# Kernel optimization log

Hardware: AMD Instinct MI355X
Metric: run time of the kernel (lower is better)

Reference implementation:

```python
import jax, jax.numpy as jnp
import numpy as np

N_NODES = 349525  # complete 4-ary tree, depth 10: (4**10 - 1) / 3
X_SIZE = 128
H_SIZE = 128


def setup_inputs() -> dict:
    key = jax.random.key(0)
    ks = jax.random.split(key, 6)
    s = 0.05  # keep gates out of saturation
    return {
        "x": jax.random.normal(ks[0], (N_NODES, X_SIZE), jnp.float32),
        "W_iou": jax.random.normal(ks[1], (X_SIZE, 3 * H_SIZE), jnp.float32) * s,
        "U_iou": jax.random.normal(ks[2], (H_SIZE, 3 * H_SIZE), jnp.float32) * s,
        "b_iou": jnp.zeros((3 * H_SIZE,), jnp.float32),
        "W_f": jax.random.normal(ks[3], (X_SIZE, H_SIZE), jnp.float32) * s,
        "U_f": jax.random.normal(ks[4], (H_SIZE, H_SIZE), jnp.float32) * s,
        "b_f": jnp.zeros((H_SIZE,), jnp.float32),
        "depth": 10,
        "branching": 4,
    }


def _apply_node(iou, c_sum):
    # apply_node_func: i,o,u gates then cell/hidden update
    i, o, u = jnp.split(iou, 3, axis=-1)
    c = jax.nn.sigmoid(i) * jnp.tanh(u) + c_sum
    h = jax.nn.sigmoid(o) * jnp.tanh(c)
    return h, c


def reference(x, W_iou, U_iou, b_iou, W_f, U_f, b_f, depth, branching):
    # Nodes are in BFS order of a complete `branching`-ary forest-tree;
    # level l occupies [off[l], off[l+1]) and the children of level l are
    # exactly level l+1 (contiguous, `branching` per parent).
    H = b_f.shape[-1]
    off = [(branching ** l - 1) // (branching - 1) for l in range(depth + 1)]

    node_iou = x @ W_iou + b_iou  # [N, 3H]  (W_iou(x) + b_iou)
    node_f = x @ W_f + b_f        # [N, H]   (W_f(x) + b_f)

    h_levels = [None] * depth
    c_levels = [None] * depth

    # Leaves: mailbox empty -> h_tilda = 0, c = 0
    s, e = off[depth - 1], off[depth]
    h, c = _apply_node(node_iou[s:e], jnp.zeros((e - s, H), x.dtype))
    h_levels[depth - 1], c_levels[depth - 1] = h, c

    # Bottom-up topological propagation
    for l in range(depth - 2, -1, -1):
        s, e = off[l], off[l + 1]
        nl = e - s
        ch_h = h_levels[l + 1].reshape(nl, branching, H)  # mailbox['h']
        ch_c = c_levels[l + 1].reshape(nl, branching, H)  # mailbox['c']
        h_tilda = ch_h.sum(axis=1)
        # f = sigmoid(U_f(mailbox.h) + node_f[:, None])
        f = jax.nn.sigmoid(jnp.einsum("nkh,hg->nkg", ch_h, U_f) + node_f[s:e][:, None, :])
        c_sum = (f * ch_c).sum(axis=1)
        iou = node_iou[s:e] + h_tilda @ U_iou
        h, c = _apply_node(iou, c_sum)
        h_levels[l], c_levels[l] = h, c

    h_all = jnp.concatenate(h_levels, axis=0)
    c_all = jnp.concatenate(c_levels, axis=0)
    return h_all, c_all
```

## Files before the change

### kernel.cpp

```cpp
#include <hip/hip_runtime.h>

#define H 128

typedef __bf16 bf16x8 __attribute__((ext_vector_type(8)));
typedef float f32x4 __attribute__((ext_vector_type(4)));

__device__ __forceinline__ float fsig(float x) { return 1.0f / (1.0f + __expf(-x)); }
__device__ __forceinline__ float ftanh(float x) {
  float ax = fabsf(x), e = __expf(-2.0f * ax);
  float t = (1.0f - e) / (1.0f + e);
  return x < 0.0f ? -t : t;
}
__device__ __forceinline__ uint2 pack4(float a, float b, float c, float d) {
  union { __bf16 h[4]; uint2 u; } r;
  r.h[0] = (__bf16)a; r.h[1] = (__bf16)b; r.h[2] = (__bf16)c; r.h[3] = (__bf16)d;
  return r.u;
}
__device__ __forceinline__ unsigned swz(unsigned row, unsigned colByte, unsigned rowBytes) {
  return (row * rowBytes + colByte) ^ ((row & 7) << 4);
}

__global__ __launch_bounds__(256)
void prep_weights(const float* __restrict__ W_iou, const float* __restrict__ U_iou,
                  const float* __restrict__ W_f, const float* __restrict__ U_f,
                  uint4* __restrict__ ws)
{
  int item = blockIdx.x * 256 + threadIdx.x;
  float v[8];
  if (item < 2048) {
    int fj = item >> 8, rem = item & 255, ks = rem >> 6, lane = rem & 63;
    int n = fj * 16 + (lane & 15), kb = ks * 32 + (lane >> 4) * 8;
    #pragma unroll
    for (int j = 0; j < 8; j++) v[j] = U_f[(kb + j) * H + n];
  } else if (item < 4096) {
    int i2 = item - 2048;
    int fj = i2 >> 8, rem = i2 & 255, ks = rem >> 6, lane = rem & 63;
    int n = fj * 16 + (lane & 15), kb = ks * 32 + (lane >> 4) * 8;
    #pragma unroll
    for (int j = 0; j < 8; j++) v[j] = W_f[(kb + j) * H + n];
  } else {
    int i2 = item - 4096;
    int fj = i2 >> 9, rem = i2 & 511, ks = rem >> 6, lane = rem & 63;
    int col = (fj >> 3) * 128 + (fj & 7) * 16 + (lane & 15);
    int kb = ks * 32 + (lane >> 4) * 8;
    #pragma unroll
    for (int j = 0; j < 8; j++) {
      int k = kb + j;
      v[j] = (k < 128) ? W_iou[k * 384 + col] : U_iou[(k - 128) * 384 + col];
    }
  }
  union { __bf16 h[8]; uint4 u; } r;
  #pragma unroll
  for (int j = 0; j < 8; j++) r.h[j] = (__bf16)v[j];
  ws[item] = r.u;
}

__global__ __launch_bounds__(256)
void leaf3(const float* __restrict__ x, const __bf16* __restrict__ iou_fmt,
           const float* __restrict__ b_iou,
           float* __restrict__ h_glob, float* __restrict__ c_glob, int leaf_start)
{
  __shared__ __align__(16) char As[64 * 256];
  const int t = threadIdx.x;
  const int m0 = leaf_start + blockIdx.x * 64;

  #pragma unroll
  for (int i = 0; i < 8; i++) {
    int idx = t + i * 256;
    int r = idx >> 5, k0 = (idx & 31) << 2;
    f32x4 v = *reinterpret_cast<const f32x4*>(&x[(size_t)(m0 + r) * H + k0]);
    *reinterpret_cast<uint2*>(As + swz(r, k0 * 2, 256)) = pack4(v.x, v.y, v.z, v.w);
  }
  __syncthreads();

  const int lane = t & 63, w = t >> 6;
  const int l15 = lane & 15, l4 = lane >> 4;

  f32x4 acc[4][3][2] = {};
  #pragma unroll
  for (int ks = 0; ks < 4; ks++) {
    bf16x8 a[4], b[3][2];
    #pragma unroll
    for (int m = 0; m < 4; m++)
      a[m] = *reinterpret_cast<const bf16x8*>(As + swz(m * 16 + l15, (ks * 32 + l4 * 8) * 2, 256));
    #pragma unroll
    for (int g = 0; g < 3; g++)
      #pragma unroll
      for (int j = 0; j < 2; j++) {
        int nf = g * 8 + 2 * w + j;
        b[g][j] = *reinterpret_cast<const bf16x8*>(iou_fmt + ((size_t)(nf * 8 + ks) * 64 + lane) * 8);
      }
    #pragma unroll
    for (int m = 0; m < 4; m++)
      #pragma unroll
      for (int g = 0; g < 3; g++)
        #pragma unroll
        for (int j = 0; j < 2; j++)
          acc[m][g][j] = __builtin_amdgcn_mfma_f32_16x16x32_bf16(a[m], b[g][j], acc[m][g][j], 0, 0, 0);
  }

  #pragma unroll
  for (int j = 0; j < 2; j++) {
    int ch = (2 * w + j) * 16 + l15;
    float bi = b_iou[ch], bo = b_iou[H + ch], bu = b_iou[2 * H + ch];
    #pragma unroll
    for (int m = 0; m < 4; m++) {
      int rowb = m * 16 + l4 * 4;
      #pragma unroll
      for (int r = 0; r < 4; r++) {
        size_t o = (size_t)(m0 + rowb + r) * H + ch;
        float c = fsig(acc[m][0][j][r] + bi) * ftanh(acc[m][2][j][r] + bu);
        float h = fsig(acc[m][1][j][r] + bo) * ftanh(c);
        h_glob[o] = h;
        c_glob[o] = c;
      }
    }
  }
}

__global__ __launch_bounds__(256)
void fused_level(const float* __restrict__ x, const __bf16* __restrict__ uf_fmt,
                 const __bf16* __restrict__ wf_fmt, const __bf16* __restrict__ iou_fmt,
                 const float* __restrict__ b_iou, const float* __restrict__ b_f,
                 float* __restrict__ h_glob, float* __restrict__ c_glob,
                 int pstart, int cstart)
{
  __shared__ __align__(16) char CH[128 * 256];
  __shared__ __align__(16) char XH[32 * 512];
  __shared__ float SFX[32][128];
  __shared__ float CSUM[32][128];
  const int t = threadIdx.x;
  const int p0 = blockIdx.x * 32;
  const int c0 = blockIdx.x * 128;

  #pragma unroll
  for (int i = 0; i < 4; i++) {
    int idx = t + i * 256;
    int p = idx >> 5, k0 = (idx & 31) << 2;
    f32x4 s = {};
    #pragma unroll
    for (int j = 0; j < 4; j++) {
      f32x4 v = *reinterpret_cast<const f32x4*>(&h_glob[(size_t)(cstart + c0 + p * 4 + j) * H + k0]);
      *reinterpret_cast<uint2*>(CH + swz(p * 4 + j, k0 * 2, 256)) = pack4(v.x, v.y, v.z, v.w);
      s += v;
    }
    *reinterpret_cast<uint2*>(XH + swz(p, (128 + k0) * 2, 512)) = pack4(s.x, s.y, s.z, s.w);
  }
  #pragma unroll
  for (int i = 0; i < 4; i++) {
    int idx = t + i * 256;
    int p = idx >> 5, k0 = (idx & 31) << 2;
    f32x4 v = *reinterpret_cast<const f32x4*>(&x[(size_t)(pstart + p0 + p) * H + k0]);
    *reinterpret_cast<uint2*>(XH + swz(p, k0 * 2, 512)) = pack4(v.x, v.y, v.z, v.w);
  }
  __syncthreads();

  const int lane = t & 63, w = t >> 6;
  const int l15 = lane & 15, l4 = lane >> 4;

  {
    f32x4 acc[2][2] = {};
    #pragma unroll
    for (int ks = 0; ks < 4; ks++) {
      bf16x8 a[2], b[2];
      #pragma unroll
      for (int m = 0; m < 2; m++)
        a[m] = *reinterpret_cast<const bf16x8*>(XH + swz(m * 16 + l15, (ks * 32 + l4 * 8) * 2, 512));
      #pragma unroll
      for (int n = 0; n < 2; n++) {
        int nf = 2 * w + n;
        b[n] = *reinterpret_cast<const bf16x8*>(wf_fmt + ((size_t)(nf * 4 + ks) * 64 + lane) * 8);
      }
      #pragma unroll
      for (int m = 0; m < 2; m++)
        #pragma unroll
        for (int n = 0; n < 2; n++)
          acc[m][n] = __builtin_amdgcn_mfma_f32_16x16x32_bf16(a[m], b[n], acc[m][n], 0, 0, 0);
    }
    #pragma unroll
    for (int m = 0; m < 2; m++)
      #pragma unroll
      for (int n = 0; n < 2; n++)
        #pragma unroll
        for (int r = 0; r < 4; r++)
          SFX[m * 16 + l4 * 4 + r][(2 * w + n) * 16 + l15] = acc[m][n][r];
  }
  __syncthreads();

  {
    f32x4 acc[2][8] = {};
    #pragma unroll
    for (int ks = 0; ks < 4; ks++) {
      bf16x8 a[2], b[8];
      #pragma unroll
      for (int m = 0; m < 2; m++)
        a[m] = *reinterpret_cast<const bf16x8*>(CH + swz(w * 32 + m * 16 + l15, (ks * 32 + l4 * 8) * 2, 256));
      #pragma unroll
      for (int n = 0; n < 8; n++)
        b[n] = *reinterpret_cast<const bf16x8*>(uf_fmt + ((size_t)(n * 4 + ks) * 64 + lane) * 8);
      #pragma unroll
      for (int m = 0; m < 2; m++)
        #pragma unroll
        for (int n = 0; n < 8; n++)
          acc[m][n] = __builtin_amdgcn_mfma_f32_16x16x32_bf16(a[m], b[n], acc[m][n], 0, 0, 0);
    }
    #pragma unroll
    for (int m = 0; m < 2; m++) {
      int rbase = w * 32 + m * 16 + l4 * 4;
      int ploc = rbase >> 2;
      #pragma unroll
      for (int n = 0; n < 8; n++) {
        int ch = n * 16 + l15;
        float sfx = SFX[ploc][ch] + b_f[ch];
        float cs = 0.0f;
        #pragma unroll
        for (int r = 0; r < 4; r++) {
          float f = fsig(acc[m][n][r] + sfx);
          cs = fmaf(f, c_glob[(size_t)(cstart + c0 + rbase + r) * H + ch], cs);
        }
        CSUM[ploc][ch] = cs;
      }
    }
  }
  __syncthreads();

  {
    f32x4 acc[2][3][2] = {};
    #pragma unroll
    for (int ks = 0; ks < 8; ks++) {
      bf16x8 a[2], b[3][2];
      #pragma unroll
      for (int m = 0; m < 2; m++)
        a[m] = *reinterpret_cast<const bf16x8*>(XH + swz(m * 16 + l15, (ks * 32 + l4 * 8) * 2, 512));
      #pragma unroll
      for (int g = 0; g < 3; g++)
        #pragma unroll
        for (int j = 0; j < 2; j++) {
          int nf = g * 8 + 2 * w + j;
          b[g][j] = *reinterpret_cast<const bf16x8*>(iou_fmt + ((size_t)(nf * 8 + ks) * 64 + lane) * 8);
        }
      #pragma unroll
      for (int m = 0; m < 2; m++)
        #pragma unroll
        for (int g = 0; g < 3; g++)
          #pragma unroll
          for (int j = 0; j < 2; j++)
            acc[m][g][j] = __builtin_amdgcn_mfma_f32_16x16x32_bf16(a[m], b[g][j], acc[m][g][j], 0, 0, 0);
    }
    #pragma unroll
    for (int j = 0; j < 2; j++) {
      int ch = (2 * w + j) * 16 + l15;
      float bi = b_iou[ch], bo = b_iou[H + ch], bu = b_iou[2 * H + ch];
      #pragma unroll
      for (int m = 0; m < 2; m++) {
        #pragma unroll
        for (int r = 0; r < 4; r++) {
          int ploc = m * 16 + l4 * 4 + r;
          float gi = acc[m][0][j][r] + bi;
          float go = acc[m][1][j][r] + bo;
          float gu = acc[m][2][j][r] + bu;
          float cs = CSUM[ploc][ch];
          float c = fsig(gi) * ftanh(gu) + cs;
          float h = fsig(go) * ftanh(c);
          size_t o = (size_t)(pstart + p0 + ploc) * H + ch;
          h_glob[o] = h;
          c_glob[o] = c;
        }
      }
    }
  }
}

#define SNR 4
#define SRP 2
#define BR 4

__global__ __launch_bounds__(256)
void small_kernel(const float* __restrict__ x,
                  const float* __restrict__ W_iou, const float* __restrict__ b_iou,
                  const float* __restrict__ U_iou, const float* __restrict__ W_f,
                  const float* __restrict__ U_f, const float* __restrict__ b_f,
                  float* __restrict__ h_out, float* __restrict__ c_out,
                  int lvl_start, int child_start, int n_lvl)
{
  __shared__ float xs[SNR][H];
  __shared__ float hs[SNR * BR][H];
  __shared__ float ht[SNR][H];
  const int t = threadIdx.x;
  const int node0 = blockIdx.x * SNR;
  const int nrows = min(SNR, n_lvl - node0);

  {
    const f32x4* xgv = reinterpret_cast<const f32x4*>(x + (size_t)(lvl_start + node0) * H);
    f32x4* xsv = reinterpret_cast<f32x4*>(&xs[0][0]);
    int total = nrows * (H / 4);
    for (int i = t; i < total; i += 256) xsv[i] = xgv[i];
  }
  {
    const f32x4* hgv = reinterpret_cast<const f32x4*>(h_out + (size_t)(child_start + node0 * BR) * H);
    f32x4* hsv = reinterpret_cast<f32x4*>(&hs[0][0]);
    int total = nrows * BR * (H / 4);
    for (int i = t; i < total; i += 256) hsv[i] = hgv[i];
  }
  __syncthreads();

  const int ch = t & (H - 1);
  const int g = t >> 7;

  float fx[SRP], ai[SRP], ao[SRP], au[SRP];
  {
    float bi = b_iou[ch], bo = b_iou[ch + H], bu = b_iou[ch + 2 * H], bf = b_f[ch];
    #pragma unroll
    for (int r = 0; r < SRP; r++) { fx[r] = bf; ai[r] = bi; ao[r] = bo; au[r] = bu; }
  }
  {
    const float* wfp = W_f + ch;
    const float* wip = W_iou + ch;
    #pragma unroll 4
    for (int k = 0; k < H; k++) {
      float wf = wfp[k * H];
      float w0 = wip[k * 384], w1 = wip[k * 384 + H], w2 = wip[k * 384 + 2 * H];
      #pragma unroll
      for (int r = 0; r < SRP; r++) {
        float xk = xs[g * SRP + r][k];
        fx[r] = fmaf(xk, wf, fx[r]);
        ai[r] = fmaf(xk, w0, ai[r]);
        ao[r] = fmaf(xk, w1, ao[r]);
        au[r] = fmaf(xk, w2, au[r]);
      }
    }
  }
  #pragma unroll
  for (int r = 0; r < SRP; r++) {
    int row = g * SRP + r;
    float s = hs[row * BR + 0][ch] + hs[row * BR + 1][ch]
            + hs[row * BR + 2][ch] + hs[row * BR + 3][ch];
    ht[row][ch] = s;
  }
  __syncthreads();

  float z[BR][SRP];
  #pragma unroll
  for (int kc = 0; kc < BR; kc++)
    #pragma unroll
    for (int r = 0; r < SRP; r++) z[kc][r] = fx[r];
  {
    const float* ufp = U_f + ch;
    #pragma unroll 4
    for (int m = 0; m < H; m++) {
      float uf = ufp[m * H];
      #pragma unroll
      for (int kc = 0; kc < BR; kc++)
        #pragma unroll
        for (int r = 0; r < SRP; r++)
          z[kc][r] = fmaf(hs[(g * SRP + r) * BR + kc][m], uf, z[kc][r]);
    }
  }
  float csum[SRP];
  #pragma unroll
  for (int r = 0; r < SRP; r++) csum[r] = 0.0f;
  #pragma unroll
  for (int kc = 0; kc < BR; kc++) {
    #pragma unroll
    for (int r = 0; r < SRP; r++) {
      size_t childnode = (size_t)child_start + (size_t)(node0 + g * SRP + r) * BR + kc;
      float f = fsig(z[kc][r]);
      csum[r] = fmaf(f, c_out[childnode * H + ch], csum[r]);
    }
  }
  {
    const float* uip = U_iou + ch;
    #pragma unroll 4
    for (int m = 0; m < H; m++) {
      float w0 = uip[m * 384], w1 = uip[m * 384 + H], w2 = uip[m * 384 + 2 * H];
      #pragma unroll
      for (int r = 0; r < SRP; r++) {
        float hm = ht[g * SRP + r][m];
        ai[r] = fmaf(hm, w0, ai[r]);
        ao[r] = fmaf(hm, w1, ao[r]);
        au[r] = fmaf(hm, w2, au[r]);
      }
    }
  }
  #pragma unroll
  for (int r = 0; r < SRP; r++) {
    int row = g * SRP + r;
    if (row < nrows) {
      float c = fsig(ai[r]) * ftanh(au[r]) + csum[r];
      float h = fsig(ao[r]) * ftanh(c);
      size_t node = (size_t)(lvl_start + node0 + row);
      h_out[node * H + ch] = h;
      c_out[node * H + ch] = c;
    }
  }
}

extern "C" void kernel_launch(void* const* d_in, const int* in_sizes, int n_in,
                              void* d_out, int out_size, void* d_ws, size_t ws_size,
                              hipStream_t stream)
{
  const float* x     = (const float*)d_in[0];
  const float* W_iou = (const float*)d_in[1];
  const float* U_iou = (const float*)d_in[2];
  const float* b_iou = (const float*)d_in[3];
  const float* W_f   = (const float*)d_in[4];
  const float* U_f   = (const float*)d_in[5];
  const float* b_f   = (const float*)d_in[6];
  const int N = 349525;

  float* h_out = (float*)d_out;
  float* c_out = h_out + (size_t)N * H;

  const __bf16* uf_fmt  = (const __bf16*)d_ws;
  const __bf16* wf_fmt  = (const __bf16*)d_ws + 16384;
  const __bf16* iou_fmt = (const __bf16*)d_ws + 32768;

  int off[11];
  off[0] = 0;
  for (int l = 1; l <= 10; l++) off[l] = off[l - 1] * 4 + 1;

  prep_weights<<<64, 256, 0, stream>>>(W_iou, U_iou, W_f, U_f, (uint4*)d_ws);

  leaf3<<<4096, 256, 0, stream>>>(x, iou_fmt, b_iou, h_out, c_out, off[9]);

  for (int l = 8; l >= 5; l--) {
    int n_par = off[l + 1] - off[l];
    fused_level<<<n_par / 32, 256, 0, stream>>>(x, uf_fmt, wf_fmt, iou_fmt, b_iou, b_f,
                                                h_out, c_out, off[l], off[l + 1]);
  }

  for (int l = 4; l >= 0; l--) {
    int s = off[l], e = off[l + 1];
    int n = e - s;
    int grid = (n + SNR - 1) / SNR;
    small_kernel<<<grid, 256, 0, stream>>>(x, W_iou, b_iou, U_iou, W_f, U_f, b_f,
                                           h_out, c_out, s, e, n);
  }
}
```

Baseline: 409.2 us.

## Pipeline leaf tiles with double-buffered LDS, merge shared buffers, fast reciprocals

The leaf kernel now processes four 64-row tiles per block, prefetching the next tile's x into registers while computing the current one and double-buffering LDS. fused_level merges its SFX and CSUM shared arrays into one buffer to cut LDS use and allow more blocks per CU. Sigmoid and tanh use hardware approximate reciprocals instead of divides. Level 4 moves from the small kernel to fused_level. Risks are reduced precision in the gates and fewer blocks for the leaf level.

```diff
diff --git a/kernel.cpp b/kernel.cpp
--- a/kernel.cpp
+++ b/kernel.cpp
@@ -5,10 +5,12 @@
 typedef __bf16 bf16x8 __attribute__((ext_vector_type(8)));
 typedef float f32x4 __attribute__((ext_vector_type(4)));
 
-__device__ __forceinline__ float fsig(float x) { return 1.0f / (1.0f + __expf(-x)); }
+__device__ __forceinline__ float fsig(float x) {
+  return __builtin_amdgcn_rcpf(1.0f + __expf(-x));
+}
 __device__ __forceinline__ float ftanh(float x) {
   float ax = fabsf(x), e = __expf(-2.0f * ax);
-  float t = (1.0f - e) / (1.0f + e);
+  float t = (1.0f - e) * __builtin_amdgcn_rcpf(1.0f + e);
   return x < 0.0f ? -t : t;
 }
 __device__ __forceinline__ uint2 pack4(float a, float b, float c, float d) {
@@ -55,66 +57,88 @@
   ws[item] = r.u;
 }
 
-__global__ __launch_bounds__(256)
-void leaf3(const float* __restrict__ x, const __bf16* __restrict__ iou_fmt,
+#define LTILES 4
+__global__ __launch_bounds__(256, 3)
+void leaf4(const float* __restrict__ x, const __bf16* __restrict__ iou_fmt,
            const float* __restrict__ b_iou,
            float* __restrict__ h_glob, float* __restrict__ c_glob, int leaf_start)
 {
-  __shared__ __align__(16) char As[64 * 256];
+  __shared__ __align__(16) char As[2][64 * 256];
   const int t = threadIdx.x;
-  const int m0 = leaf_start + blockIdx.x * 64;
-
-  #pragma unroll
-  for (int i = 0; i < 8; i++) {
-    int idx = t + i * 256;
-    int r = idx >> 5, k0 = (idx & 31) << 2;
-    f32x4 v = *reinterpret_cast<const f32x4*>(&x[(size_t)(m0 + r) * H + k0]);
-    *reinterpret_cast<uint2*>(As + swz(r, k0 * 2, 256)) = pack4(v.x, v.y, v.z, v.w);
-  }
-  __syncthreads();
-
+  const int m00 = leaf_start + blockIdx.x * (64 * LTILES);
   const int lane = t & 63, w = t >> 6;
   const int l15 = lane & 15, l4 = lane >> 4;
-
-  f32x4 acc[4][3][2] = {};
-  #pragma unroll
-  for (int ks = 0; ks < 4; ks++) {
-    bf16x8 a[4], b[3][2];
-    #pragma unroll
-    for (int m = 0; m < 4; m++)
-      a[m] = *reinterpret_cast<const bf16x8*>(As + swz(m * 16 + l15, (ks * 32 + l4 * 8) * 2, 256));
-    #pragma unroll
-    for (int g = 0; g < 3; g++)
-      #pragma unroll
-      for (int j = 0; j < 2; j++) {
-        int nf = g * 8 + 2 * w + j;
-        b[g][j] = *reinterpret_cast<const bf16x8*>(iou_fmt + ((size_t)(nf * 8 + ks) * 64 + lane) * 8);
-      }
-    #pragma unroll
-    for (int m = 0; m < 4; m++)
+  const int r_st = t >> 5;
+  const int k_st = (t & 31) << 2;
+
+  f32x4 rg[8];
+  #pragma unroll
+  for (int i = 0; i < 8; i++)
+    rg[i] = *reinterpret_cast<const f32x4*>(&x[(size_t)(m00 + r_st + i * 8) * H + k_st]);
+  #pragma unroll
+  for (int i = 0; i < 8; i++)
+    *reinterpret_cast<uint2*>(As[0] + swz(r_st + i * 8, k_st * 2, 256)) =
+        pack4(rg[i].x, rg[i].y, rg[i].z, rg[i].w);
+  __syncthreads();
+
+  for (int tt = 0; tt < LTILES; tt++) {
+    if (tt + 1 < LTILES) {
+      #pragma unroll
+      for (int i = 0; i < 8; i++)
+        rg[i] = *reinterpret_cast<const f32x4*>(
+            &x[(size_t)(m00 + (tt + 1) * 64 + r_st + i * 8) * H + k_st]);
+    }
+    const char* A = As[tt & 1];
+    const int m0 = m00 + tt * 64;
+
+    f32x4 acc[4][3][2] = {};
+    #pragma unroll
+    for (int ks = 0; ks < 4; ks++) {
+      bf16x8 a[4], b[3][2];
+      #pragma unroll
+      for (int m = 0; m < 4; m++)
+        a[m] = *reinterpret_cast<const bf16x8*>(A + swz(m * 16 + l15, (ks * 32 + l4 * 8) * 2, 256));
       #pragma unroll
       for (int g = 0; g < 3; g++)
         #pragma unroll
-        for (int j = 0; j < 2; j++)
-          acc[m][g][j] = __builtin_amdgcn_mfma_f32_16x16x32_bf16(a[m], b[g][j], acc[m][g][j], 0, 0, 0);
-  }
-
-  #pragma unroll
-  for (int j = 0; j < 2; j++) {
-    int ch = (2 * w + j) * 16 + l15;
-    float bi = b_iou[ch], bo = b_iou[H + ch], bu = b_iou[2 * H + ch];
-    #pragma unroll
-    for (int m = 0; m < 4; m++) {
-      int rowb = m * 16 + l4 * 4;
-      #pragma unroll
-      for (int r = 0; r < 4; r++) {
-        size_t o = (size_t)(m0 + rowb + r) * H + ch;
-        float c = fsig(acc[m][0][j][r] + bi) * ftanh(acc[m][2][j][r] + bu);
-        float h = fsig(acc[m][1][j][r] + bo) * ftanh(c);
-        h_glob[o] = h;
-        c_glob[o] = c;
-      }
-    }
+        for (int j = 0; j < 2; j++) {
+          int nf = g * 8 + 2 * w + j;
+          b[g][j] = *reinterpret_cast<const bf16x8*>(iou_fmt + ((size_t)(nf * 8 + ks) * 64 + lane) * 8);
+        }
+      #pragma unroll
+      for (int m = 0; m < 4; m++)
+        #pragma unroll
+        for (int g = 0; g < 3; g++)
+          #pragma unroll
+          for (int j = 0; j < 2; j++)
+            acc[m][g][j] = __builtin_amdgcn_mfma_f32_16x16x32_bf16(a[m], b[g][j], acc[m][g][j], 0, 0, 0);
+    }
+
+    #pragma unroll
+    for (int j = 0; j < 2; j++) {
+      int ch = (2 * w + j) * 16 + l15;
+      float bi = b_iou[ch], bo = b_iou[H + ch], bu = b_iou[2 * H + ch];
+      #pragma unroll
+      for (int m = 0; m < 4; m++) {
+        int rowb = m * 16 + l4 * 4;
+        #pragma unroll
+        for (int r = 0; r < 4; r++) {
+          size_t o = (size_t)(m0 + rowb + r) * H + ch;
+          float c = fsig(acc[m][0][j][r] + bi) * ftanh(acc[m][2][j][r] + bu);
+          float h = fsig(acc[m][1][j][r] + bo) * ftanh(c);
+          h_glob[o] = h;
+          c_glob[o] = c;
+        }
+      }
+    }
+
+    if (tt + 1 < LTILES) {
+      #pragma unroll
+      for (int i = 0; i < 8; i++)
+        *reinterpret_cast<uint2*>(As[(tt + 1) & 1] + swz(r_st + i * 8, k_st * 2, 256)) =
+            pack4(rg[i].x, rg[i].y, rg[i].z, rg[i].w);
+    }
+    __syncthreads();
   }
 }
 
@@ -127,8 +151,7 @@
 {
   __shared__ __align__(16) char CH[128 * 256];
   __shared__ __align__(16) char XH[32 * 512];
-  __shared__ float SFX[32][128];
-  __shared__ float CSUM[32][128];
+  __shared__ float SC[32][128];
   const int t = threadIdx.x;
   const int p0 = blockIdx.x * 32;
   const int c0 = blockIdx.x * 128;
@@ -183,7 +206,7 @@
       for (int n = 0; n < 2; n++)
         #pragma unroll
         for (int r = 0; r < 4; r++)
-          SFX[m * 16 + l4 * 4 + r][(2 * w + n) * 16 + l15] = acc[m][n][r];
+          SC[m * 16 + l4 * 4 + r][(2 * w + n) * 16 + l15] = acc[m][n][r];
   }
   __syncthreads();
 
@@ -211,14 +234,14 @@
       #pragma unroll
       for (int n = 0; n < 8; n++) {
         int ch = n * 16 + l15;
-        float sfx = SFX[ploc][ch] + b_f[ch];
+        float sfx = SC[ploc][ch] + b_f[ch];
         float cs = 0.0f;
         #pragma unroll
         for (int r = 0; r < 4; r++) {
           float f = fsig(acc[m][n][r] + sfx);
           cs = fmaf(f, c_glob[(size_t)(cstart + c0 + rbase + r) * H + ch], cs);
         }
-        CSUM[ploc][ch] = cs;
+        SC[ploc][ch] = cs;
       }
     }
   }
@@ -259,7 +282,7 @@
           float gi = acc[m][0][j][r] + bi;
           float go = acc[m][1][j][r] + bo;
           float gu = acc[m][2][j][r] + bu;
-          float cs = CSUM[ploc][ch];
+          float cs = SC[ploc][ch];
           float c = fsig(gi) * ftanh(gu) + cs;
           float h = fsig(go) * ftanh(c);
           size_t o = (size_t)(pstart + p0 + ploc) * H + ch;
@@ -421,15 +444,15 @@
 
   prep_weights<<<64, 256, 0, stream>>>(W_iou, U_iou, W_f, U_f, (uint4*)d_ws);
 
-  leaf3<<<4096, 256, 0, stream>>>(x, iou_fmt, b_iou, h_out, c_out, off[9]);
-
-  for (int l = 8; l >= 5; l--) {
+  leaf4<<<1024, 256, 0, stream>>>(x, iou_fmt, b_iou, h_out, c_out, off[9]);
+
+  for (int l = 8; l >= 4; l--) {
     int n_par = off[l + 1] - off[l];
     fused_level<<<n_par / 32, 256, 0, stream>>>(x, uf_fmt, wf_fmt, iou_fmt, b_iou, b_f,
                                                 h_out, c_out, off[l], off[l + 1]);
   }
 
-  for (int l = 4; l >= 0; l--) {
+  for (int l = 3; l >= 0; l--) {
     int s = off[l], e = off[l + 1];
     int n = e - s;
     int grid = (n + SNR - 1) / SNR;
```

Result: slower. 558.1 us (+36.4%).

## Trim leaf registers, merge LDS buffers, use rcp intrinsics, fuse level four

Applied to the files above, without the earlier changes.

The leaf kernel now loops over the two column halves without unrolling, which cuts the live MFMA accumulators by half and should lower register pressure and raise occupancy. In fused_level, the SFX and CSUM shared buffers are merged into one array, freeing 16 KB of LDS per block. The divisions in sigmoid and tanh are replaced by the hardware reciprocal intrinsic, which is slightly less accurate. Level 4 now runs through the MFMA fused_level kernel instead of the scalar small kernel, though that level launches only 8 blocks.

```diff
diff --git a/kernel.cpp b/kernel.cpp
--- a/kernel.cpp
+++ b/kernel.cpp
@@ -5,10 +5,12 @@
 typedef __bf16 bf16x8 __attribute__((ext_vector_type(8)));
 typedef float f32x4 __attribute__((ext_vector_type(4)));
 
-__device__ __forceinline__ float fsig(float x) { return 1.0f / (1.0f + __expf(-x)); }
+__device__ __forceinline__ float fsig(float x) {
+  return __builtin_amdgcn_rcpf(1.0f + __expf(-x));
+}
 __device__ __forceinline__ float ftanh(float x) {
   float ax = fabsf(x), e = __expf(-2.0f * ax);
-  float t = (1.0f - e) / (1.0f + e);
+  float t = (1.0f - e) * __builtin_amdgcn_rcpf(1.0f + e);
   return x < 0.0f ? -t : t;
 }
 __device__ __forceinline__ uint2 pack4(float a, float b, float c, float d) {
@@ -56,7 +58,7 @@
 }
 
 __global__ __launch_bounds__(256)
-void leaf3(const float* __restrict__ x, const __bf16* __restrict__ iou_fmt,
+void leaf5(const float* __restrict__ x, const __bf16* __restrict__ iou_fmt,
            const float* __restrict__ b_iou,
            float* __restrict__ h_glob, float* __restrict__ c_glob, int leaf_start)
 {
@@ -76,31 +78,27 @@
   const int lane = t & 63, w = t >> 6;
   const int l15 = lane & 15, l4 = lane >> 4;
 
-  f32x4 acc[4][3][2] = {};
-  #pragma unroll
-  for (int ks = 0; ks < 4; ks++) {
-    bf16x8 a[4], b[3][2];
-    #pragma unroll
-    for (int m = 0; m < 4; m++)
-      a[m] = *reinterpret_cast<const bf16x8*>(As + swz(m * 16 + l15, (ks * 32 + l4 * 8) * 2, 256));
-    #pragma unroll
-    for (int g = 0; g < 3; g++)
-      #pragma unroll
-      for (int j = 0; j < 2; j++) {
+  #pragma unroll 1
+  for (int j = 0; j < 2; j++) {
+    f32x4 acc[4][3] = {};
+    #pragma unroll
+    for (int ks = 0; ks < 4; ks++) {
+      bf16x8 a[4], b[3];
+      #pragma unroll
+      for (int m = 0; m < 4; m++)
+        a[m] = *reinterpret_cast<const bf16x8*>(As + swz(m * 16 + l15, (ks * 32 + l4 * 8) * 2, 256));
+      #pragma unroll
+      for (int g = 0; g < 3; g++) {
         int nf = g * 8 + 2 * w + j;
-        b[g][j] = *reinterpret_cast<const bf16x8*>(iou_fmt + ((size_t)(nf * 8 + ks) * 64 + lane) * 8);
-      }
-    #pragma unroll
-    for (int m = 0; m < 4; m++)
-      #pragma unroll
-      for (int g = 0; g < 3; g++)
-        #pragma unroll
-        for (int j = 0; j < 2; j++)
-          acc[m][g][j] = __builtin_amdgcn_mfma_f32_16x16x32_bf16(a[m], b[g][j], acc[m][g][j], 0, 0, 0);
-  }
-
-  #pragma unroll
-  for (int j = 0; j < 2; j++) {
+        b[g] = *reinterpret_cast<const bf16x8*>(iou_fmt + ((size_t)(nf * 8 + ks) * 64 + lane) * 8);
+      }
+      #pragma unroll
+      for (int m = 0; m < 4; m++)
+        #pragma unroll
+        for (int g = 0; g < 3; g++)
+          acc[m][g] = __builtin_amdgcn_mfma_f32_16x16x32_bf16(a[m], b[g], acc[m][g], 0, 0, 0);
+    }
+
     int ch = (2 * w + j) * 16 + l15;
     float bi = b_iou[ch], bo = b_iou[H + ch], bu = b_iou[2 * H + ch];
     #pragma unroll
@@ -109,8 +107,8 @@
       #pragma unroll
       for (int r = 0; r < 4; r++) {
         size_t o = (size_t)(m0 + rowb + r) * H + ch;
-        float c = fsig(acc[m][0][j][r] + bi) * ftanh(acc[m][2][j][r] + bu);
-        float h = fsig(acc[m][1][j][r] + bo) * ftanh(c);
+        float c = fsig(acc[m][0][r] + bi) * ftanh(acc[m][2][r] + bu);
+        float h = fsig(acc[m][1][r] + bo) * ftanh(c);
         h_glob[o] = h;
         c_glob[o] = c;
       }
@@ -127,8 +125,7 @@
 {
   __shared__ __align__(16) char CH[128 * 256];
   __shared__ __align__(16) char XH[32 * 512];
-  __shared__ float SFX[32][128];
-  __shared__ float CSUM[32][128];
+  __shared__ float SC[32][128];
   const int t = threadIdx.x;
   const int p0 = blockIdx.x * 32;
   const int c0 = blockIdx.x * 128;
@@ -183,7 +180,7 @@
       for (int n = 0; n < 2; n++)
         #pragma unroll
         for (int r = 0; r < 4; r++)
-          SFX[m * 16 + l4 * 4 + r][(2 * w + n) * 16 + l15] = acc[m][n][r];
+          SC[m * 16 + l4 * 4 + r][(2 * w + n) * 16 + l15] = acc[m][n][r];
   }
   __syncthreads();
 
@@ -211,14 +208,14 @@
       #pragma unroll
       for (int n = 0; n < 8; n++) {
         int ch = n * 16 + l15;
-        float sfx = SFX[ploc][ch] + b_f[ch];
+        float sfx = SC[ploc][ch] + b_f[ch];
         float cs = 0.0f;
         #pragma unroll
         for (int r = 0; r < 4; r++) {
           float f = fsig(acc[m][n][r] + sfx);
           cs = fmaf(f, c_glob[(size_t)(cstart + c0 + rbase + r) * H + ch], cs);
         }
-        CSUM[ploc][ch] = cs;
+        SC[ploc][ch] = cs;
       }
     }
   }
@@ -259,7 +256,7 @@
           float gi = acc[m][0][j][r] + bi;
           float go = acc[m][1][j][r] + bo;
           float gu = acc[m][2][j][r] + bu;
-          float cs = CSUM[ploc][ch];
+          float cs = SC[ploc][ch];
           float c = fsig(gi) * ftanh(gu) + cs;
           float h = fsig(go) * ftanh(c);
           size_t o = (size_t)(pstart + p0 + ploc) * H + ch;
@@ -421,15 +418,15 @@
 
   prep_weights<<<64, 256, 0, stream>>>(W_iou, U_iou, W_f, U_f, (uint4*)d_ws);
 
-  leaf3<<<4096, 256, 0, stream>>>(x, iou_fmt, b_iou, h_out, c_out, off[9]);
-
-  for (int l = 8; l >= 5; l--) {
+  leaf5<<<4096, 256, 0, stream>>>(x, iou_fmt, b_iou, h_out, c_out, off[9]);
+
+  for (int l = 8; l >= 4; l--) {
     int n_par = off[l + 1] - off[l];
     fused_level<<<n_par / 32, 256, 0, stream>>>(x, uf_fmt, wf_fmt, iou_fmt, b_iou, b_f,
                                                 h_out, c_out, off[l], off[l + 1]);
   }
 
-  for (int l = 4; l >= 0; l--) {
+  for (int l = 3; l >= 0; l--) {
     int s = off[l], e = off[l + 1];
     int n = e - s;
     int grid = (n + SNR - 1) / SNR;
```

Measured after the change: 399.4 us. 1.02x faster.
